# Kernel optimization log

Measured on AMD Instinct MI355X. Metric: run time of the kernel, lower is better.

The kernel has to match this reference:

```python
import jax, jax.numpy as jnp
import numpy as np

S, B, I, H = 512, 8192, 3, 5  # seq, batch, input_size, hidden_size


def _uniform(key, shape, bound):
    return jax.random.uniform(key, shape, jnp.float32, -bound, bound)


def setup_inputs() -> dict:
    key = jax.random.key(0)
    ks = jax.random.split(key, 17)
    bound = 1.0 / np.sqrt(H)
    inp = {"x": jax.random.normal(ks[0], (S, B, I), jnp.float32)}
    # layer 0: in=I ; layer 1: in=2H (concat of both directions). Suffix 'r' = reverse direction.
    specs = [
        ("l0", I), ("l0r", I), ("l1", 2 * H), ("l1r", 2 * H),
    ]
    ki = 1
    for name, din in specs:
        inp[f"w_ih_{name}"] = _uniform(ks[ki], (4 * H, din), bound); ki += 1
        inp[f"w_hh_{name}"] = _uniform(ks[ki], (4 * H, H), bound); ki += 1
        inp[f"b_ih_{name}"] = _uniform(ks[ki], (4 * H,), bound); ki += 1
        inp[f"b_hh_{name}"] = _uniform(ks[ki], (4 * H,), bound); ki += 1
    return inp


def _lstm_dir(x, w_ih, w_hh, b_ih, b_hh, reverse):
    """Single-direction LSTM over x [S,B,Din] -> (hs [S,B,H], h_T [B,H], c_T [B,H])."""
    xs = x[::-1] if reverse else x
    # Precompute input contributions for all timesteps in one big matmul.
    gx = jnp.einsum('sbi,gi->sbg', xs, w_ih) + b_ih + b_hh  # [S,B,4H]
    h0 = jnp.zeros((x.shape[1], H), x.dtype)
    c0 = jnp.zeros((x.shape[1], H), x.dtype)

    def step(carry, g):
        h, c = carry
        g = g + h @ w_hh.T  # [B,4H]
        i, f, gg, o = jnp.split(g, 4, axis=-1)  # PyTorch gate order: i,f,g,o
        i = jax.nn.sigmoid(i)
        f = jax.nn.sigmoid(f)
        gg = jnp.tanh(gg)
        o = jax.nn.sigmoid(o)
        c = f * c + i * gg
        h = o * jnp.tanh(c)
        return (h, c), h

    (hT, cT), hs = jax.lax.scan(step, (h0, c0), gx)
    if reverse:
        hs = hs[::-1]
    return hs, hT, cT


def reference(x,
              w_ih_l0, w_hh_l0, b_ih_l0, b_hh_l0,
              w_ih_l0r, w_hh_l0r, b_ih_l0r, b_hh_l0r,
              w_ih_l1, w_hh_l1, b_ih_l1, b_hh_l1,
              w_ih_l1r, w_hh_l1r, b_ih_l1r, b_hh_l1r):
    # Layer 0 (bidirectional)
    hs0f, h0f, c0f = _lstm_dir(x, w_ih_l0, w_hh_l0, b_ih_l0, b_hh_l0, False)
    hs0b, h0b, c0b = _lstm_dir(x, w_ih_l0r, w_hh_l0r, b_ih_l0r, b_hh_l0r, True)
    out0 = jnp.concatenate([hs0f, hs0b], axis=-1)  # [S,B,2H]
    # Layer 1 (bidirectional) consumes concat of both directions
    hs1f, h1f, c1f = _lstm_dir(out0, w_ih_l1, w_hh_l1, b_ih_l1, b_hh_l1, False)
    hs1b, h1b, c1b = _lstm_dir(out0, w_ih_l1r, w_hh_l1r, b_ih_l1r, b_hh_l1r, True)
    output = jnp.concatenate([hs1f, hs1b], axis=-1)  # [S,B,2H]
    # PyTorch h_n/c_n layout: [num_layers*num_directions, B, H] ordered (l0 fwd, l0 bwd, l1 fwd, l1 bwd)
    h_n = jnp.stack([h0f, h0b, h1f, h1b], axis=0)
    c_n = jnp.stack([c0f, c0b, c1f, c1b], axis=0)
    return output, h_n, c_n
```

## Files before the change

### kernel.cpp

```cpp
#include <hip/hip_runtime.h>


constexpr int S_ = 512;
constexpr int B_ = 8192;
constexpr int NROW = 16384;

constexpr float L2E  = 1.4426950408889634f;
constexpr float T2E  = 2.8853900817779268f;
constexpr float IT2E = 0.34657359027997264f;

typedef _Float16 v2h __attribute__((ext_vector_type(2)));

__device__ __forceinline__ float dot2h(v2h a, v2h b, float c) {
#if __has_builtin(__builtin_amdgcn_fdot2)
    return __builtin_amdgcn_fdot2(a, b, c, false);
#else
    return fmaf((float)a[0], (float)b[0], fmaf((float)a[1], (float)b[1], c));
#endif
}

__device__ __forceinline__ float rcp_(float x) { return __builtin_amdgcn_rcpf(x); }

__device__ __forceinline__ float exp2_(float x) {
#if __has_builtin(__builtin_amdgcn_exp2f)
    return __builtin_amdgcn_exp2f(x);
#else
    return exp2f(x);
#endif
}

__device__ __forceinline__ void sbar() { __builtin_amdgcn_sched_barrier(0); }

__device__ __forceinline__ float bperm(int bidx, float v) {
    return __int_as_float(__builtin_amdgcn_ds_bpermute(bidx, __float_as_int(v)));
}

__device__ __forceinline__ unsigned pkh(float a, float b) {
    auto t = __builtin_amdgcn_cvt_pkrtz(a, b);
    unsigned q; __builtin_memcpy(&q, &t, 4); return q;
}

__global__ __launch_bounds__(64) __attribute__((amdgpu_waves_per_eu(1, 2)))
void lstm_layer0(
    const float* __restrict__ x,
    const float* __restrict__ wih_f, const float* __restrict__ whh_f,
    const float* __restrict__ bih_f, const float* __restrict__ bhh_f,
    const float* __restrict__ wih_r, const float* __restrict__ whh_r,
    const float* __restrict__ bih_r, const float* __restrict__ bhh_r,
    unsigned short* __restrict__ ws,
    float* __restrict__ outbase)
{
    const int l64 = threadIdx.x & 63;
    int r = l64 / 5; r = (r > 11) ? 11 : r;
    const int u   = l64 - r * 5;
    const int uc  = (u < 5) ? u : 4;
    const int gid = blockIdx.x * 12 + r;
    const bool valid = gid < NROW;
    const int dir = (gid >> 13) & 1;
    const int b   = gid & 8191;
    const bool stw = valid && (u < 3);
    const bool st  = valid && (u < 5);

    int bidx[5];
#pragma unroll
    for (int k = 0; k < 5; k++) bidx[k] = (r * 5 + k) * 4;

    const float* __restrict__ wih = dir ? wih_r : wih_f;
    const float* __restrict__ whh = dir ? whh_r : whh_f;
    const float* __restrict__ bih = dir ? bih_r : bih_f;
    const float* __restrict__ bhh = dir ? bhh_r : bhh_f;

    const int rows[4] = {uc, 5 + uc, 10 + uc, 15 + uc};
    const float scl[4] = {-L2E, -L2E, T2E, -L2E};
    float WX[4][3], WH[4][5], BS[4];
#pragma unroll
    for (int gi = 0; gi < 4; gi++) {
        const int rr = rows[gi]; const float sc = scl[gi];
#pragma unroll
        for (int i = 0; i < 3; i++) WX[gi][i] = wih[rr * 3 + i] * sc;
#pragma unroll
        for (int k = 0; k < 5; k++) WH[gi][k] = whh[rr * 5 + k] * sc;
        BS[gi] = (bih[rr] + bhh[rr]) * sc;
    }

    float h[5] = {0.f, 0.f, 0.f, 0.f, 0.f};
    float cp = 0.f, hu_last = 0.f;

    const int t0 = dir ? (S_ - 1) : 0;
    const float* xp = x + ((size_t)t0 * B_ + b) * 3;
    unsigned short* wp = ws + (size_t)dir * ((size_t)S_ * B_ * 6)
                            + ((size_t)t0 * B_ + b) * 6;
    const ptrdiff_t xst = dir ? -(ptrdiff_t)3 * B_ : (ptrdiff_t)3 * B_;
    const ptrdiff_t wst = dir ? -(ptrdiff_t)6 * B_ : (ptrdiff_t)6 * B_;

    auto step = [&](const float (&xin)[3], unsigned short* wpp) {
        float a0 = BS[0], a1 = BS[1], a2 = BS[2], a3 = BS[3];
#pragma unroll
        for (int i = 0; i < 3; i++) {
            a0 = fmaf(WX[0][i], xin[i], a0);
            a1 = fmaf(WX[1][i], xin[i], a1);
            a2 = fmaf(WX[2][i], xin[i], a2);
            a3 = fmaf(WX[3][i], xin[i], a3);
        }
#pragma unroll
        for (int k = 0; k < 5; k++) {
            a0 = fmaf(WH[0][k], h[k], a0);
            a1 = fmaf(WH[1][k], h[k], a1);
            a2 = fmaf(WH[2][k], h[k], a2);
            a3 = fmaf(WH[3][k], h[k], a3);
        }
        const float ig = rcp_(1.0f + exp2_(a0));
        const float fg = rcp_(1.0f + exp2_(a1));
        const float g2 = fmaf(-2.0f * T2E, rcp_(1.0f + exp2_(a2)), T2E);
        const float og = rcp_(1.0f + exp2_(a3));
        cp = fmaf(fg, cp, ig * g2);
        const float th = fmaf(-2.0f, rcp_(1.0f + exp2_(cp)), 1.0f);
        const float hu = og * th;
        hu_last = hu;
#pragma unroll
        for (int k = 0; k < 5; k++) h[k] = bperm(bidx[k], hu);
        const unsigned q0 = pkh(h[0], h[1]);
        const unsigned q1 = pkh(h[2], h[3]);
        const unsigned q2 = pkh(h[4], 0.0f);
        unsigned qs = q0;
        qs = (u == 1) ? q1 : qs;
        qs = (u == 2) ? q2 : qs;
        if (stw) ((unsigned*)wpp)[u] = qs;
    };

    auto ld = [&](float (&buf)[3]) {
        __builtin_memcpy(&buf[0], xp, 12);
        xp += xst;
        sbar();
    };

    float x0[3], x1[3], x2[3], x3[3], x4[3], x5[3], x6[3], x7[3];
    ld(x0); ld(x1); ld(x2); ld(x3); ld(x4); ld(x5); ld(x6); ld(x7);

#pragma unroll 1
    for (int s = 0; s < S_ - 8; s += 8) {
        step(x0, wp); wp += wst; ld(x0);
        step(x1, wp); wp += wst; ld(x1);
        step(x2, wp); wp += wst; ld(x2);
        step(x3, wp); wp += wst; ld(x3);
        step(x4, wp); wp += wst; ld(x4);
        step(x5, wp); wp += wst; ld(x5);
        step(x6, wp); wp += wst; ld(x6);
        step(x7, wp); wp += wst; ld(x7);
    }
    step(x0, wp); wp += wst;
    step(x1, wp); wp += wst;
    step(x2, wp); wp += wst;
    step(x3, wp); wp += wst;
    step(x4, wp); wp += wst;
    step(x5, wp); wp += wst;
    step(x6, wp); wp += wst;
    step(x7, wp);

    const size_t OUTE = (size_t)S_ * B_ * 10;
    float* hn = outbase + OUTE + ((size_t)dir * B_ + b) * 5;
    float* cn = hn + (size_t)4 * B_ * 5;
    if (st) { hn[uc] = hu_last; cn[uc] = cp * IT2E; }
}

__global__ __launch_bounds__(64) __attribute__((amdgpu_waves_per_eu(1, 2)))
void lstm_layer1(
    const unsigned short* __restrict__ ws,
    const float* __restrict__ wih_f, const float* __restrict__ whh_f,
    const float* __restrict__ bih_f, const float* __restrict__ bhh_f,
    const float* __restrict__ wih_r, const float* __restrict__ whh_r,
    const float* __restrict__ bih_r, const float* __restrict__ bhh_r,
    float* __restrict__ outbase)
{
    const int l64 = threadIdx.x & 63;
    int r = l64 / 5; r = (r > 11) ? 11 : r;
    const int u   = l64 - r * 5;
    const int uc  = (u < 5) ? u : 4;
    const int gid = blockIdx.x * 12 + r;
    const bool valid = gid < NROW;
    const int dir = (gid >> 13) & 1;
    const int b   = gid & 8191;
    const bool st = valid && (u < 5);

    int bidx[5];
#pragma unroll
    for (int k = 0; k < 5; k++) bidx[k] = (r * 5 + k) * 4;

    const float* __restrict__ wih = dir ? wih_r : wih_f;
    const float* __restrict__ whh = dir ? whh_r : whh_f;
    const float* __restrict__ bih = dir ? bih_r : bih_f;
    const float* __restrict__ bhh = dir ? bhh_r : bhh_f;

    const int rows[4] = {uc, 5 + uc, 10 + uc, 15 + uc};
    const float scl[4] = {-L2E, -L2E, T2E, -L2E};
    v2h WX[4][6];
    float WH[4][5], BS[4];
#pragma unroll
    for (int gi = 0; gi < 4; gi++) {
        const int rr = rows[gi]; const float sc = scl[gi];
#pragma unroll
        for (int p = 0; p < 6; p++) {
            const int i0 = (p < 3) ? 2 * p : 2 * p - 1;
            const bool pad = (p == 2) || (p == 5);
            const float w0 = wih[rr * 10 + i0] * sc;
            const float w1 = pad ? 0.f : wih[rr * 10 + i0 + 1] * sc;
            WX[gi][p] = (v2h){(_Float16)w0, (_Float16)w1};
        }
#pragma unroll
        for (int k = 0; k < 5; k++) WH[gi][k] = whh[rr * 5 + k] * sc;
        BS[gi] = (bih[rr] + bhh[rr]) * sc;
    }

    float h[5] = {0.f, 0.f, 0.f, 0.f, 0.f};
    float cp = 0.f, hu_last = 0.f;

    const int t0 = dir ? (S_ - 1) : 0;
    const unsigned short* rpf = ws + ((size_t)t0 * B_ + b) * 6;
    const unsigned short* rpb = rpf + (size_t)S_ * B_ * 6;
    float* op = outbase + ((size_t)t0 * B_ + b) * 10 + dir * 5;
    const ptrdiff_t rst = dir ? -(ptrdiff_t)6 * B_ : (ptrdiff_t)6 * B_;
    const ptrdiff_t ost = dir ? -(ptrdiff_t)10 * B_ : (ptrdiff_t)10 * B_;

    auto step = [&](const v2h (&xin)[6], float* opp) {
        float a0 = BS[0], a1 = BS[1], a2 = BS[2], a3 = BS[3];
#pragma unroll
        for (int p = 0; p < 6; p++) {
            a0 = dot2h(xin[p], WX[0][p], a0);
            a1 = dot2h(xin[p], WX[1][p], a1);
            a2 = dot2h(xin[p], WX[2][p], a2);
            a3 = dot2h(xin[p], WX[3][p], a3);
        }
#pragma unroll
        for (int k = 0; k < 5; k++) {
            a0 = fmaf(WH[0][k], h[k], a0);
            a1 = fmaf(WH[1][k], h[k], a1);
            a2 = fmaf(WH[2][k], h[k], a2);
            a3 = fmaf(WH[3][k], h[k], a3);
        }
        const float ig = rcp_(1.0f + exp2_(a0));
        const float fg = rcp_(1.0f + exp2_(a1));
        const float g2 = fmaf(-2.0f * T2E, rcp_(1.0f + exp2_(a2)), T2E);
        const float og = rcp_(1.0f + exp2_(a3));
        cp = fmaf(fg, cp, ig * g2);
        const float th = fmaf(-2.0f, rcp_(1.0f + exp2_(cp)), 1.0f);
        const float hu = og * th;
        hu_last = hu;
        if (st) opp[u] = hu;
#pragma unroll
        for (int k = 0; k < 5; k++) h[k] = bperm(bidx[k], hu);
    };

    auto ld = [&](v2h (&buf)[6]) {
        __builtin_memcpy(&buf[0], rpf, 12);
        __builtin_memcpy(&buf[3], rpb, 12);
        rpf += rst; rpb += rst;
        sbar();
    };

    v2h x0[6], x1[6], x2[6], x3[6];
    ld(x0); ld(x1); ld(x2); ld(x3);

#pragma unroll 1
    for (int s = 0; s < S_ - 4; s += 4) {
        step(x0, op); op += ost; ld(x0);
        step(x1, op); op += ost; ld(x1);
        step(x2, op); op += ost; ld(x2);
        step(x3, op); op += ost; ld(x3);
    }
    step(x0, op); op += ost;
    step(x1, op); op += ost;
    step(x2, op); op += ost;
    step(x3, op);

    const size_t OUTE = (size_t)S_ * B_ * 10;
    float* hn = outbase + OUTE + ((size_t)(2 + dir) * B_ + b) * 5;
    float* cn = hn + (size_t)4 * B_ * 5;
    if (st) { hn[uc] = hu_last; cn[uc] = cp * IT2E; }
}

extern "C" void kernel_launch(void* const* d_in, const int* in_sizes, int n_in,
                              void* d_out, int out_size, void* d_ws, size_t ws_size,
                              hipStream_t stream) {
    const float* x       = (const float*)d_in[0];
    const float* wih_l0  = (const float*)d_in[1];
    const float* whh_l0  = (const float*)d_in[2];
    const float* bih_l0  = (const float*)d_in[3];
    const float* bhh_l0  = (const float*)d_in[4];
    const float* wih_l0r = (const float*)d_in[5];
    const float* whh_l0r = (const float*)d_in[6];
    const float* bih_l0r = (const float*)d_in[7];
    const float* bhh_l0r = (const float*)d_in[8];
    const float* wih_l1  = (const float*)d_in[9];
    const float* whh_l1  = (const float*)d_in[10];
    const float* bih_l1  = (const float*)d_in[11];
    const float* bhh_l1  = (const float*)d_in[12];
    const float* wih_l1r = (const float*)d_in[13];
    const float* whh_l1r = (const float*)d_in[14];
    const float* bih_l1r = (const float*)d_in[15];
    const float* bhh_l1r = (const float*)d_in[16];

    float* out = (float*)d_out;
    unsigned short* ws = (unsigned short*)d_ws;

    dim3 grid(1366), block(64);
    lstm_layer0<<<grid, block, 0, stream>>>(x,
        wih_l0, whh_l0, bih_l0, bhh_l0,
        wih_l0r, whh_l0r, bih_l0r, bhh_l0r,
        ws, out);
    lstm_layer1<<<grid, block, 0, stream>>>(ws,
        wih_l1, whh_l1, bih_l1, bhh_l1,
        wih_l1r, whh_l1r, bih_l1r, bhh_l1r,
        out);
}
```

Measured before the change: 325.2 us.

## Pair fwd/bwd layer-1 rows per block and write full 10-float output rows

Layer 1 now places the forward and backward directions of the same batch element in one wave. Each direction stashes its first 256 hidden outputs in LDS (fp16, 208 steps) or in a global spill buffer. It then writes complete 10-float output rows, both directions' halves, during the second half of the sequence. This replaces the strided 5-float half-row writes with contiguous full-row stores, which should improve write coalescing. The cost is LDS use, an extra global temp buffer, fp16 rounding of the stored half of the outputs, and extra per-step loads.

```diff
diff --git a/kernel.cpp b/kernel.cpp
--- a/kernel.cpp
+++ b/kernel.cpp
@@ -4,6 +4,10 @@
 constexpr int S_ = 512;
 constexpr int B_ = 8192;
 constexpr int NROW = 16384;
+
+constexpr int GD1  = 1366;
+constexpr int TL   = 208;
+constexpr int GSTR = GD1 * 64;
 
 constexpr float L2E  = 1.4426950408889634f;
 constexpr float T2E  = 2.8853900817779268f;
@@ -38,6 +42,15 @@
 __device__ __forceinline__ unsigned pkh(float a, float b) {
     auto t = __builtin_amdgcn_cvt_pkrtz(a, b);
     unsigned q; __builtin_memcpy(&q, &t, 4); return q;
+}
+
+__device__ __forceinline__ unsigned short f2h(float x) {
+    _Float16 h = (_Float16)x;
+    unsigned short s; __builtin_memcpy(&s, &h, 2); return s;
+}
+
+__device__ __forceinline__ float h2f(unsigned short s) {
+    _Float16 h; __builtin_memcpy(&h, &s, 2); return (float)h;
 }
 
 __global__ __launch_bounds__(64) __attribute__((amdgpu_waves_per_eu(1, 2)))
@@ -170,17 +183,24 @@
     const float* __restrict__ bih_f, const float* __restrict__ bhh_f,
     const float* __restrict__ wih_r, const float* __restrict__ whh_r,
     const float* __restrict__ bih_r, const float* __restrict__ bhh_r,
-    float* __restrict__ outbase)
+    float* __restrict__ outbase,
+    unsigned short* __restrict__ gtemp)
 {
+    __shared__ unsigned short lt[TL * 60];
+
     const int l64 = threadIdx.x & 63;
     int r = l64 / 5; r = (r > 11) ? 11 : r;
     const int u   = l64 - r * 5;
     const int uc  = (u < 5) ? u : 4;
-    const int gid = blockIdx.x * 12 + r;
-    const bool valid = gid < NROW;
-    const int dir = (gid >> 13) & 1;
-    const int b   = gid & 8191;
+    const int rm  = (r < 6) ? r : r - 6;
+    const int dir = (r >= 6) ? 1 : 0;
+    const int braw = blockIdx.x * 6 + rm;
+    const bool valid = braw < B_;
+    const int b   = valid ? braw : (B_ - 1);
     const bool st = valid && (u < 5);
+    const bool lw = (l64 < 60);
+    const int dir5 = dir * 5;
+    const int pslot = (dir ? (r - 6) : (r + 6)) * 5 + uc;
 
     int bidx[5];
 #pragma unroll
@@ -217,11 +237,15 @@
     const int t0 = dir ? (S_ - 1) : 0;
     const unsigned short* rpf = ws + ((size_t)t0 * B_ + b) * 6;
     const unsigned short* rpb = rpf + (size_t)S_ * B_ * 6;
-    float* op = outbase + ((size_t)t0 * B_ + b) * 10 + dir * 5;
+    float* op = outbase + ((size_t)(dir ? 255 : 256) * B_ + b) * 10;
     const ptrdiff_t rst = dir ? -(ptrdiff_t)6 * B_ : (ptrdiff_t)6 * B_;
     const ptrdiff_t ost = dir ? -(ptrdiff_t)10 * B_ : (ptrdiff_t)10 * B_;
 
-    auto step = [&](const v2h (&xin)[6], float* opp) {
+    unsigned short* gw = gtemp + (size_t)blockIdx.x * 64 + l64;
+    const unsigned short* gr = gtemp + (size_t)47 * GSTR
+                                     + (size_t)blockIdx.x * 64 + pslot;
+
+    auto core = [&](const v2h (&xin)[6]) -> float {
         float a0 = BS[0], a1 = BS[1], a2 = BS[2], a3 = BS[3];
 #pragma unroll
         for (int p = 0; p < 6; p++) {
@@ -245,9 +269,37 @@
         const float th = fmaf(-2.0f, rcp_(1.0f + exp2_(cp)), 1.0f);
         const float hu = og * th;
         hu_last = hu;
-        if (st) opp[u] = hu;
+        return hu;
+    };
+
+    auto bcast = [&](float hu) {
 #pragma unroll
         for (int k = 0; k < 5; k++) h[k] = bperm(bidx[k], hu);
+    };
+
+    auto step1L = [&](const v2h (&xin)[6], int t) {
+        const float hu = core(xin);
+        if (lw) lt[t * 60 + l64] = f2h(hu);
+        bcast(hu);
+    };
+    auto step1G = [&](const v2h (&xin)[6]) {
+        const float hu = core(xin);
+        *gw = f2h(hu);
+        gw += GSTR;
+        bcast(hu);
+    };
+    auto step2G = [&](const v2h (&xin)[6], float* opp) {
+        const float pv = h2f(*gr);
+        gr -= GSTR;
+        const float hu = core(xin);
+        if (st) { opp[dir5 + u] = hu; opp[5 - dir5 + u] = pv; }
+        bcast(hu);
+    };
+    auto step2L = [&](const v2h (&xin)[6], int t, float* opp) {
+        const float pv = h2f(lt[(511 - t) * 60 + pslot]);
+        const float hu = core(xin);
+        if (st) { opp[dir5 + u] = hu; opp[5 - dir5 + u] = pv; }
+        bcast(hu);
     };
 
     auto ld = [&](v2h (&buf)[6]) {
@@ -261,16 +313,37 @@
     ld(x0); ld(x1); ld(x2); ld(x3);
 
 #pragma unroll 1
-    for (int s = 0; s < S_ - 4; s += 4) {
-        step(x0, op); op += ost; ld(x0);
-        step(x1, op); op += ost; ld(x1);
-        step(x2, op); op += ost; ld(x2);
-        step(x3, op); op += ost; ld(x3);
-    }
-    step(x0, op); op += ost;
-    step(x1, op); op += ost;
-    step(x2, op); op += ost;
-    step(x3, op);
+    for (int t = 0; t < TL; t += 4) {
+        step1L(x0, t + 0); ld(x0);
+        step1L(x1, t + 1); ld(x1);
+        step1L(x2, t + 2); ld(x2);
+        step1L(x3, t + 3); ld(x3);
+    }
+#pragma unroll 1
+    for (int t = TL; t < 256; t += 4) {
+        step1G(x0); ld(x0);
+        step1G(x1); ld(x1);
+        step1G(x2); ld(x2);
+        step1G(x3); ld(x3);
+    }
+#pragma unroll 1
+    for (int t = 256; t < 304; t += 4) {
+        step2G(x0, op); op += ost; ld(x0);
+        step2G(x1, op); op += ost; ld(x1);
+        step2G(x2, op); op += ost; ld(x2);
+        step2G(x3, op); op += ost; ld(x3);
+    }
+#pragma unroll 1
+    for (int t = 304; t < 508; t += 4) {
+        step2L(x0, t + 0, op); op += ost; ld(x0);
+        step2L(x1, t + 1, op); op += ost; ld(x1);
+        step2L(x2, t + 2, op); op += ost; ld(x2);
+        step2L(x3, t + 3, op); op += ost; ld(x3);
+    }
+    step2L(x0, 508, op); op += ost;
+    step2L(x1, 509, op); op += ost;
+    step2L(x2, 510, op); op += ost;
+    step2L(x3, 511, op);
 
     const size_t OUTE = (size_t)S_ * B_ * 10;
     float* hn = outbase + OUTE + ((size_t)(2 + dir) * B_ + b) * 5;
@@ -301,14 +374,16 @@
 
     float* out = (float*)d_out;
     unsigned short* ws = (unsigned short*)d_ws;
-
-    dim3 grid(1366), block(64);
-    lstm_layer0<<<grid, block, 0, stream>>>(x,
+    unsigned short* gtemp = ws + (size_t)2 * S_ * B_ * 6;
+
+    dim3 grid0(1366), block(64);
+    lstm_layer0<<<grid0, block, 0, stream>>>(x,
         wih_l0, whh_l0, bih_l0, bhh_l0,
         wih_l0r, whh_l0r, bih_l0r, bhh_l0r,
         ws, out);
-    lstm_layer1<<<grid, block, 0, stream>>>(ws,
+    dim3 grid1(GD1);
+    lstm_layer1<<<grid1, block, 0, stream>>>(ws,
         wih_l1, whh_l1, bih_l1, bhh_l1,
         wih_l1r, whh_l1r, bih_l1r, bhh_l1r,
-        out);
-}
+        out, gtemp);
+}
```

Result: no change. 330.8 us (+1.7%).

## Remap layer-1 LSTM lanes to gate-parallel layout with fused bidirectional output staging

Applied to the files above, without the earlier changes.

Layer 1 now assigns each lane one gate (i, f, g or o) for five hidden units of a batch row, replacing the old mapping of one hidden unit per lane. Gates are exchanged with quad DPP broadcasts instead of ds_bpermute, and forward and reverse rows share a wave. Each direction stages its first-half hidden states as fp16 in LDS (with a global spill for the remainder) so the partner direction can write full 10-wide output rows in the second half. Block IDs for both kernels are also swizzled across XCDs. The aim is to cut cross-lane shuffle cost and scattered output stores, at the price of more register pressure, LDS use and fp16 rounding of the staged outputs.

```diff
diff --git a/kernel.cpp b/kernel.cpp
--- a/kernel.cpp
+++ b/kernel.cpp
@@ -4,6 +4,9 @@
 constexpr int S_ = 512;
 constexpr int B_ = 8192;
 constexpr int NROW = 16384;
+
+constexpr int GD1 = 1024;
+constexpr int TL  = 208;
 
 constexpr float L2E  = 1.4426950408889634f;
 constexpr float T2E  = 2.8853900817779268f;
@@ -35,9 +38,30 @@
     return __int_as_float(__builtin_amdgcn_ds_bpermute(bidx, __float_as_int(v)));
 }
 
+template<int L>
+__device__ __forceinline__ float qb(float v) {
+    return __int_as_float(__builtin_amdgcn_update_dpp(
+        0, __float_as_int(v), L * 0x55, 0xF, 0xF, false));
+}
+
 __device__ __forceinline__ unsigned pkh(float a, float b) {
     auto t = __builtin_amdgcn_cvt_pkrtz(a, b);
     unsigned q; __builtin_memcpy(&q, &t, 4); return q;
+}
+
+__device__ __forceinline__ unsigned short f2h(float x) {
+    _Float16 h = (_Float16)x;
+    unsigned short s; __builtin_memcpy(&s, &h, 2); return s;
+}
+
+__device__ __forceinline__ float h2f(unsigned short s) {
+    _Float16 h; __builtin_memcpy(&h, &s, 2); return (float)h;
+}
+
+__device__ __forceinline__ int xswz1366(int bid) {
+    const int xcd = bid & 7, loc = bid >> 3;
+    const int base = (xcd < 6) ? xcd * 171 : 1026 + (xcd - 6) * 170;
+    return base + loc;
 }
 
 __global__ __launch_bounds__(64) __attribute__((amdgpu_waves_per_eu(1, 2)))
@@ -54,7 +78,8 @@
     int r = l64 / 5; r = (r > 11) ? 11 : r;
     const int u   = l64 - r * 5;
     const int uc  = (u < 5) ? u : 4;
-    const int gid = blockIdx.x * 12 + r;
+    const int bsw = xswz1366((int)blockIdx.x);
+    const int gid = bsw * 12 + r;
     const bool valid = gid < NROW;
     const int dir = (gid >> 13) & 1;
     const int b   = gid & 8191;
@@ -170,85 +195,59 @@
     const float* __restrict__ bih_f, const float* __restrict__ bhh_f,
     const float* __restrict__ wih_r, const float* __restrict__ whh_r,
     const float* __restrict__ bih_r, const float* __restrict__ bhh_r,
-    float* __restrict__ outbase)
+    float* __restrict__ outbase,
+    unsigned short* __restrict__ gtemp)
 {
+    __shared__ unsigned lt[TL * 48];
+
     const int l64 = threadIdx.x & 63;
-    int r = l64 / 5; r = (r > 11) ? 11 : r;
-    const int u   = l64 - r * 5;
-    const int uc  = (u < 5) ? u : 4;
-    const int gid = blockIdx.x * 12 + r;
-    const bool valid = gid < NROW;
-    const int dir = (gid >> 13) & 1;
-    const int b   = gid & 8191;
-    const bool st = valid && (u < 5);
-
-    int bidx[5];
-#pragma unroll
-    for (int k = 0; k < 5; k++) bidx[k] = (r * 5 + k) * 4;
+    const int bid = (int)blockIdx.x;
+    const int bsw = (bid & 7) * 128 + (bid >> 3);
+    const int q   = l64 >> 2;
+    const int g   = l64 & 3;
+    const int dir = q >> 3;
+    const int qm  = q & 7;
+    const int b   = bsw * 8 + qm;
+    const int pq  = q ^ 8;
+    const bool c2sel = (g == 0) ? (dir == 0) : (dir == 1);
 
     const float* __restrict__ wih = dir ? wih_r : wih_f;
     const float* __restrict__ whh = dir ? whh_r : whh_f;
     const float* __restrict__ bih = dir ? bih_r : bih_f;
     const float* __restrict__ bhh = dir ? bhh_r : bhh_f;
 
-    const int rows[4] = {uc, 5 + uc, 10 + uc, 15 + uc};
-    const float scl[4] = {-L2E, -L2E, T2E, -L2E};
-    v2h WX[4][6];
-    float WH[4][5], BS[4];
-#pragma unroll
-    for (int gi = 0; gi < 4; gi++) {
-        const int rr = rows[gi]; const float sc = scl[gi];
+    const float scl = (g == 2) ? T2E : -L2E;
+    const float GM  = (g == 2) ? (-2.0f * T2E) : 1.0f;
+    const float GB  = (g == 2) ? T2E : 0.0f;
+
+    v2h  WX[5][6];
+    float WH[5][5], BS[5];
+#pragma unroll
+    for (int u = 0; u < 5; u++) {
+        const int rr = g * 5 + u;
 #pragma unroll
         for (int p = 0; p < 6; p++) {
             const int i0 = (p < 3) ? 2 * p : 2 * p - 1;
             const bool pad = (p == 2) || (p == 5);
-            const float w0 = wih[rr * 10 + i0] * sc;
-            const float w1 = pad ? 0.f : wih[rr * 10 + i0 + 1] * sc;
-            WX[gi][p] = (v2h){(_Float16)w0, (_Float16)w1};
-        }
-#pragma unroll
-        for (int k = 0; k < 5; k++) WH[gi][k] = whh[rr * 5 + k] * sc;
-        BS[gi] = (bih[rr] + bhh[rr]) * sc;
+            const float w0 = wih[rr * 10 + i0] * scl;
+            const float w1 = pad ? 0.f : wih[rr * 10 + i0 + 1] * scl;
+            WX[u][p] = (v2h){(_Float16)w0, (_Float16)w1};
+        }
+#pragma unroll
+        for (int k = 0; k < 5; k++) WH[u][k] = whh[rr * 5 + k] * scl;
+        BS[u] = (bih[rr] + bhh[rr]) * scl;
     }
 
-    float h[5] = {0.f, 0.f, 0.f, 0.f, 0.f};
-    float cp = 0.f, hu_last = 0.f;
+    float h[5]  = {0.f, 0.f, 0.f, 0.f, 0.f};
+    float cp[5] = {0.f, 0.f, 0.f, 0.f, 0.f};
 
     const int t0 = dir ? (S_ - 1) : 0;
     const unsigned short* rpf = ws + ((size_t)t0 * B_ + b) * 6;
     const unsigned short* rpb = rpf + (size_t)S_ * B_ * 6;
-    float* op = outbase + ((size_t)t0 * B_ + b) * 10 + dir * 5;
     const ptrdiff_t rst = dir ? -(ptrdiff_t)6 * B_ : (ptrdiff_t)6 * B_;
+    float* A  = outbase + ((size_t)(dir ? 255 : 256) * B_ + b) * 10 + g;
+    float* A2 = outbase + ((size_t)(dir ? 255 : 256) * B_ + b) * 10 + ((g == 0) ? 4 : 9);
     const ptrdiff_t ost = dir ? -(ptrdiff_t)10 * B_ : (ptrdiff_t)10 * B_;
-
-    auto step = [&](const v2h (&xin)[6], float* opp) {
-        float a0 = BS[0], a1 = BS[1], a2 = BS[2], a3 = BS[3];
-#pragma unroll
-        for (int p = 0; p < 6; p++) {
-            a0 = dot2h(xin[p], WX[0][p], a0);
-            a1 = dot2h(xin[p], WX[1][p], a1);
-            a2 = dot2h(xin[p], WX[2][p], a2);
-            a3 = dot2h(xin[p], WX[3][p], a3);
-        }
-#pragma unroll
-        for (int k = 0; k < 5; k++) {
-            a0 = fmaf(WH[0][k], h[k], a0);
-            a1 = fmaf(WH[1][k], h[k], a1);
-            a2 = fmaf(WH[2][k], h[k], a2);
-            a3 = fmaf(WH[3][k], h[k], a3);
-        }
-        const float ig = rcp_(1.0f + exp2_(a0));
-        const float fg = rcp_(1.0f + exp2_(a1));
-        const float g2 = fmaf(-2.0f * T2E, rcp_(1.0f + exp2_(a2)), T2E);
-        const float og = rcp_(1.0f + exp2_(a3));
-        cp = fmaf(fg, cp, ig * g2);
-        const float th = fmaf(-2.0f, rcp_(1.0f + exp2_(cp)), 1.0f);
-        const float hu = og * th;
-        hu_last = hu;
-        if (st) opp[u] = hu;
-#pragma unroll
-        for (int k = 0; k < 5; k++) h[k] = bperm(bidx[k], hu);
-    };
 
     auto ld = [&](v2h (&buf)[6]) {
         __builtin_memcpy(&buf[0], rpf, 12);
@@ -256,26 +255,112 @@
         rpf += rst; rpb += rst;
         sbar();
     };
+    auto dots = [&](const v2h (&xin)[6], float (&a)[5]) {
+#pragma unroll
+        for (int u = 0; u < 5; u++) {
+            float t = BS[u];
+#pragma unroll
+            for (int p = 0; p < 6; p++) t = dot2h(xin[p], WX[u][p], t);
+            a[u] = t;
+        }
+    };
+    auto finish = [&](float (&a)[5]) {
+#pragma unroll
+        for (int u = 0; u < 5; u++) {
+#pragma unroll
+            for (int k = 0; k < 5; k++) a[u] = fmaf(WH[u][k], h[k], a[u]);
+        }
+        float gv[5];
+#pragma unroll
+        for (int u = 0; u < 5; u++)
+            gv[u] = fmaf(GM, rcp_(1.0f + exp2_(a[u])), GB);
+#pragma unroll
+        for (int u = 0; u < 5; u++) {
+            const float ig = qb<0>(gv[u]);
+            const float fg = qb<1>(gv[u]);
+            const float gg = qb<2>(gv[u]);
+            const float og = qb<3>(gv[u]);
+            cp[u] = fmaf(fg, cp[u], ig * gg);
+            const float th = fmaf(-2.0f, rcp_(1.0f + exp2_(cp[u])), 1.0f);
+            h[u] = og * th;
+        }
+    };
+    auto hsel = [&]() -> float {
+        return (g == 0) ? h[0] : (g == 1) ? h[1] : (g == 2) ? h[2] : h[3];
+    };
+
+    unsigned* ltw = lt + q * 3 + g;
+    auto s1L = [&](v2h (&xb)[6]) {
+        float a[5]; dots(xb, a); ld(xb); finish(a);
+        const unsigned p0 = pkh(h[0], h[1]);
+        const unsigned p1 = pkh(h[2], h[3]);
+        const unsigned p2 = pkh(h[4], 0.0f);
+        unsigned qs = (g == 1) ? p1 : p0; qs = (g == 2) ? p2 : qs;
+        if (g < 3) *ltw = qs;
+        ltw += 48;
+    };
+    unsigned short* gsw = gtemp + (size_t)bid * (48 * 80) + q * 5 + g;
+    auto s1G = [&](v2h (&xb)[6]) {
+        float a[5]; dots(xb, a); ld(xb); finish(a);
+        *gsw = f2h(hsel());
+        if (g == 0) gsw[4] = f2h(h[4]);
+        gsw += 80;
+    };
+    auto outst = [&](float pvg, float pv4) {
+        const float hg = hsel();
+        A[0] = dir ? pvg : hg;
+        A[5] = dir ? hg : pvg;
+        if (g < 2) A2[0] = c2sel ? h[4] : pv4;
+        A += ost; A2 += ost;
+    };
+    const unsigned short* grd = gtemp + (size_t)bid * (48 * 80)
+                                      + (size_t)47 * 80 + pq * 5;
+    auto s2G = [&](v2h (&xb)[6]) {
+        const float pvg = h2f(grd[g]);
+        const float pv4 = h2f(grd[4]);
+        grd -= 80;
+        float a[5]; dots(xb, a); ld(xb); finish(a);
+        outst(pvg, pv4);
+    };
+    const unsigned short* lrd = (const unsigned short*)lt
+                              + (size_t)(TL - 1) * 96 + pq * 6;
+    auto s2L = [&](v2h (&xb)[6]) {
+        const float pvg = h2f(lrd[g]);
+        const float pv4 = h2f(lrd[4]);
+        lrd -= 96;
+        float a[5]; dots(xb, a); ld(xb); finish(a);
+        outst(pvg, pv4);
+    };
+    auto s2Ln = [&](v2h (&xb)[6]) {
+        const float pvg = h2f(lrd[g]);
+        const float pv4 = h2f(lrd[4]);
+        lrd -= 96;
+        float a[5]; dots(xb, a); finish(a);
+        outst(pvg, pv4);
+    };
 
     v2h x0[6], x1[6], x2[6], x3[6];
     ld(x0); ld(x1); ld(x2); ld(x3);
 
 #pragma unroll 1
-    for (int s = 0; s < S_ - 4; s += 4) {
-        step(x0, op); op += ost; ld(x0);
-        step(x1, op); op += ost; ld(x1);
-        step(x2, op); op += ost; ld(x2);
-        step(x3, op); op += ost; ld(x3);
-    }
-    step(x0, op); op += ost;
-    step(x1, op); op += ost;
-    step(x2, op); op += ost;
-    step(x3, op);
+    for (int t = 0; t < TL; t += 4) { s1L(x0); s1L(x1); s1L(x2); s1L(x3); }
+#pragma unroll 1
+    for (int t = TL; t < 256; t += 4) { s1G(x0); s1G(x1); s1G(x2); s1G(x3); }
+    asm volatile("s_waitcnt vmcnt(0)" ::: "memory");
+#pragma unroll 1
+    for (int t = 256; t < 304; t += 4) { s2G(x0); s2G(x1); s2G(x2); s2G(x3); }
+#pragma unroll 1
+    for (int t = 304; t < 508; t += 4) { s2L(x0); s2L(x1); s2L(x2); s2L(x3); }
+    s2Ln(x0); s2Ln(x1); s2Ln(x2); s2Ln(x3);
 
     const size_t OUTE = (size_t)S_ * B_ * 10;
     float* hn = outbase + OUTE + ((size_t)(2 + dir) * B_ + b) * 5;
     float* cn = hn + (size_t)4 * B_ * 5;
-    if (st) { hn[uc] = hu_last; cn[uc] = cp * IT2E; }
+    const float hg = hsel();
+    const float cg = ((g == 0) ? cp[0] : (g == 1) ? cp[1] :
+                      (g == 2) ? cp[2] : cp[3]) * IT2E;
+    hn[g] = hg; cn[g] = cg;
+    if (g == 0) { hn[4] = h[4]; cn[4] = cp[4] * IT2E; }
 }
 
 extern "C" void kernel_launch(void* const* d_in, const int* in_sizes, int n_in,
@@ -301,14 +386,16 @@
 
     float* out = (float*)d_out;
     unsigned short* ws = (unsigned short*)d_ws;
-
-    dim3 grid(1366), block(64);
-    lstm_layer0<<<grid, block, 0, stream>>>(x,
+    unsigned short* gtemp = ws + (size_t)2 * S_ * B_ * 6;
+
+    dim3 grid0(1366), block(64);
+    lstm_layer0<<<grid0, block, 0, stream>>>(x,
         wih_l0, whh_l0, bih_l0, bhh_l0,
         wih_l0r, whh_l0r, bih_l0r, bhh_l0r,
         ws, out);
-    lstm_layer1<<<grid, block, 0, stream>>>(ws,
+    dim3 grid1(GD1);
+    lstm_layer1<<<grid1, block, 0, stream>>>(ws,
         wih_l1, whh_l1, bih_l1, bhh_l1,
         wih_l1r, whh_l1r, bih_l1r, bhh_l1r,
-        out);
-}
+        out, gtemp);
+}
```

Measured after the change: 341.9 us. +5.2%, slower.

## Restructure layer-1 LSTM as paired-lane units with LDS-staged output interleave

Applied to the files above, without the earlier changes.

Layer 1 is remapped so each pair of lanes owns one (batch, direction) sequence. One lane computes the i/g gates and the other the f/o gates for all 5 hidden units, and they exchange values through a DPP swap instead of five ds_bpermute calls per step. Forward and reverse sequences for the same batch share a block. During the first half of the sequence, results are stashed in LDS (with a small global spill past 240 steps), so each lane can write a contiguous 20-byte row holding both directions' hidden state in the second half. This removes the 5-of-64 wasted-lane layout and the scattered 4-byte stores, at the cost of a large LDS footprint, more registers per lane, and a single wave per EU.

```diff
diff --git a/kernel.cpp b/kernel.cpp
--- a/kernel.cpp
+++ b/kernel.cpp
@@ -4,6 +4,9 @@
 constexpr int S_ = 512;
 constexpr int B_ = 8192;
 constexpr int NROW = 16384;
+
+constexpr int GD1 = 512;
+constexpr int TL1 = 240;
 
 constexpr float L2E  = 1.4426950408889634f;
 constexpr float T2E  = 2.8853900817779268f;
@@ -35,9 +38,23 @@
     return __int_as_float(__builtin_amdgcn_ds_bpermute(bidx, __float_as_int(v)));
 }
 
+__device__ __forceinline__ float dsw(float v) {
+    return __int_as_float(__builtin_amdgcn_update_dpp(
+        0, __float_as_int(v), 0xB1, 0xF, 0xF, false));
+}
+
 __device__ __forceinline__ unsigned pkh(float a, float b) {
     auto t = __builtin_amdgcn_cvt_pkrtz(a, b);
     unsigned q; __builtin_memcpy(&q, &t, 4); return q;
+}
+
+__device__ __forceinline__ unsigned short f2h(float x) {
+    _Float16 h = (_Float16)x;
+    unsigned short s; __builtin_memcpy(&s, &h, 2); return s;
+}
+
+__device__ __forceinline__ float h2f(unsigned short s) {
+    _Float16 h; __builtin_memcpy(&h, &s, 2); return (float)h;
 }
 
 __global__ __launch_bounds__(64) __attribute__((amdgpu_waves_per_eu(1, 2)))
@@ -163,92 +180,74 @@
     if (st) { hn[uc] = hu_last; cn[uc] = cp * IT2E; }
 }
 
-__global__ __launch_bounds__(64) __attribute__((amdgpu_waves_per_eu(1, 2)))
+__global__ __launch_bounds__(64) __attribute__((amdgpu_waves_per_eu(1)))
 void lstm_layer1(
     const unsigned short* __restrict__ ws,
     const float* __restrict__ wih_f, const float* __restrict__ whh_f,
     const float* __restrict__ bih_f, const float* __restrict__ bhh_f,
     const float* __restrict__ wih_r, const float* __restrict__ whh_r,
     const float* __restrict__ bih_r, const float* __restrict__ bhh_r,
-    float* __restrict__ outbase)
+    float* __restrict__ outbase,
+    unsigned short* __restrict__ gtemp)
 {
+    __shared__ unsigned       ltA[TL1 * 64];
+    __shared__ unsigned short ltB[TL1 * 32];
+
     const int l64 = threadIdx.x & 63;
-    int r = l64 / 5; r = (r > 11) ? 11 : r;
-    const int u   = l64 - r * 5;
-    const int uc  = (u < 5) ? u : 4;
-    const int gid = blockIdx.x * 12 + r;
-    const bool valid = gid < NROW;
-    const int dir = (gid >> 13) & 1;
-    const int b   = gid & 8191;
-    const bool st = valid && (u < 5);
-
-    int bidx[5];
-#pragma unroll
-    for (int k = 0; k < 5; k++) bidx[k] = (r * 5 + k) * 4;
+    const int bid = (int)blockIdx.x;
+    const int bsw = (bid & 7) * 64 + (bid >> 3);
+    const int par = l64 & 1;
+    const int k   = l64 >> 1;
+    const int dir = k >> 4;
+    const int b   = bsw * 16 + (k & 15);
+    const int pk  = k ^ 16;
 
     const float* __restrict__ wih = dir ? wih_r : wih_f;
     const float* __restrict__ whh = dir ? whh_r : whh_f;
     const float* __restrict__ bih = dir ? bih_r : bih_f;
     const float* __restrict__ bhh = dir ? bhh_r : bhh_f;
 
-    const int rows[4] = {uc, 5 + uc, 10 + uc, 15 + uc};
-    const float scl[4] = {-L2E, -L2E, T2E, -L2E};
-    v2h WX[4][6];
-    float WH[4][5], BS[4];
-#pragma unroll
-    for (int gi = 0; gi < 4; gi++) {
-        const int rr = rows[gi]; const float sc = scl[gi];
-#pragma unroll
-        for (int p = 0; p < 6; p++) {
-            const int i0 = (p < 3) ? 2 * p : 2 * p - 1;
-            const bool pad = (p == 2) || (p == 5);
-            const float w0 = wih[rr * 10 + i0] * sc;
-            const float w1 = pad ? 0.f : wih[rr * 10 + i0 + 1] * sc;
-            WX[gi][p] = (v2h){(_Float16)w0, (_Float16)w1};
-        }
-#pragma unroll
-        for (int k = 0; k < 5; k++) WH[gi][k] = whh[rr * 5 + k] * sc;
-        BS[gi] = (bih[rr] + bhh[rr]) * sc;
-    }
-
-    float h[5] = {0.f, 0.f, 0.f, 0.f, 0.f};
-    float cp = 0.f, hu_last = 0.f;
+    const int G0 = par ? 2 : 0, G1 = par ? 3 : 1;
+    const float s0 = par ? T2E : -L2E;
+    const float GM0 = par ? (-2.0f * T2E) : 1.0f;
+    const float GB0 = par ? T2E : 0.0f;
+
+    v2h  WX[10][6];
+    float WH[10][5], BS[10];
+#pragma unroll
+    for (int u = 0; u < 5; u++) {
+        const int rr0 = G0 * 5 + u, rr1 = G1 * 5 + u;
+#pragma unroll
+        for (int q = 0; q < 6; q++) {
+            const int i0 = (q < 3) ? 2 * q : 2 * q - 1;
+            const bool pad = (q == 2) || (q == 5);
+            const float a0 = wih[rr0 * 10 + i0] * s0;
+            const float a1 = pad ? 0.f : wih[rr0 * 10 + i0 + 1] * s0;
+            WX[u][q] = (v2h){(_Float16)a0, (_Float16)a1};
+            const float b0 = wih[rr1 * 10 + i0] * (-L2E);
+            const float b1 = pad ? 0.f : wih[rr1 * 10 + i0 + 1] * (-L2E);
+            WX[5 + u][q] = (v2h){(_Float16)b0, (_Float16)b1};
+        }
+#pragma unroll
+        for (int kk = 0; kk < 5; kk++) {
+            WH[u][kk]     = whh[rr0 * 5 + kk] * s0;
+            WH[5 + u][kk] = whh[rr1 * 5 + kk] * (-L2E);
+        }
+        BS[u]     = (bih[rr0] + bhh[rr0]) * s0;
+        BS[5 + u] = (bih[rr1] + bhh[rr1]) * (-L2E);
+    }
+
+    float h[5]  = {0.f, 0.f, 0.f, 0.f, 0.f};
+    float cp[5] = {0.f, 0.f, 0.f, 0.f, 0.f};
 
     const int t0 = dir ? (S_ - 1) : 0;
     const unsigned short* rpf = ws + ((size_t)t0 * B_ + b) * 6;
     const unsigned short* rpb = rpf + (size_t)S_ * B_ * 6;
-    float* op = outbase + ((size_t)t0 * B_ + b) * 10 + dir * 5;
     const ptrdiff_t rst = dir ? -(ptrdiff_t)6 * B_ : (ptrdiff_t)6 * B_;
+    float* op = outbase + ((size_t)(dir ? 255 : 256) * B_ + b) * 10
+                        + (par ? (5 - dir * 5) : dir * 5);
     const ptrdiff_t ost = dir ? -(ptrdiff_t)10 * B_ : (ptrdiff_t)10 * B_;
-
-    auto step = [&](const v2h (&xin)[6], float* opp) {
-        float a0 = BS[0], a1 = BS[1], a2 = BS[2], a3 = BS[3];
-#pragma unroll
-        for (int p = 0; p < 6; p++) {
-            a0 = dot2h(xin[p], WX[0][p], a0);
-            a1 = dot2h(xin[p], WX[1][p], a1);
-            a2 = dot2h(xin[p], WX[2][p], a2);
-            a3 = dot2h(xin[p], WX[3][p], a3);
-        }
-#pragma unroll
-        for (int k = 0; k < 5; k++) {
-            a0 = fmaf(WH[0][k], h[k], a0);
-            a1 = fmaf(WH[1][k], h[k], a1);
-            a2 = fmaf(WH[2][k], h[k], a2);
-            a3 = fmaf(WH[3][k], h[k], a3);
-        }
-        const float ig = rcp_(1.0f + exp2_(a0));
-        const float fg = rcp_(1.0f + exp2_(a1));
-        const float g2 = fmaf(-2.0f * T2E, rcp_(1.0f + exp2_(a2)), T2E);
-        const float og = rcp_(1.0f + exp2_(a3));
-        cp = fmaf(fg, cp, ig * g2);
-        const float th = fmaf(-2.0f, rcp_(1.0f + exp2_(cp)), 1.0f);
-        const float hu = og * th;
-        hu_last = hu;
-        if (st) opp[u] = hu;
-#pragma unroll
-        for (int k = 0; k < 5; k++) h[k] = bperm(bidx[k], hu);
-    };
+    unsigned short* gsp = gtemp + (size_t)bid * (16 * 160);
 
     auto ld = [&](v2h (&buf)[6]) {
         __builtin_memcpy(&buf[0], rpf, 12);
@@ -257,25 +256,121 @@
         sbar();
     };
 
+    float A[10];
+    auto dots = [&](const v2h (&xin)[6]) {
+#pragma unroll
+        for (int j = 0; j < 10; j++) {
+            float t = BS[j];
+#pragma unroll
+            for (int q = 0; q < 6; q++) t = dot2h(xin[q], WX[j][q], t);
+            A[j] = t;
+        }
+    };
+    auto finish = [&]() {
+#pragma unroll
+        for (int j = 0; j < 10; j++) {
+#pragma unroll
+            for (int kk = 0; kk < 5; kk++) A[j] = fmaf(WH[j][kk], h[kk], A[j]);
+        }
+        float v0[5], v1[5], z0[5], z1[5];
+#pragma unroll
+        for (int u = 0; u < 5; u++) {
+            v0[u] = fmaf(GM0, rcp_(1.0f + exp2_(A[u])), GB0);
+            v1[u] = rcp_(1.0f + exp2_(A[5 + u]));
+        }
+#pragma unroll
+        for (int u = 0; u < 5; u++) { z0[u] = dsw(v0[u]); z1[u] = dsw(v1[u]); }
+#pragma unroll
+        for (int u = 0; u < 5; u++) {
+            const float F = par ? z1[u] : v1[u];
+            const float O = par ? v1[u] : z1[u];
+            cp[u] = fmaf(F, cp[u], v0[u] * z0[u]);
+            const float th = fmaf(-2.0f, rcp_(1.0f + exp2_(cp[u])), 1.0f);
+            h[u] = O * th;
+        }
+    };
+
+    auto outst = [&](float p0, float p1, float p2, float p3, float p4) {
+        float buf[5];
+        buf[0] = par ? p0 : h[0];
+        buf[1] = par ? p1 : h[1];
+        buf[2] = par ? p2 : h[2];
+        buf[3] = par ? p3 : h[3];
+        buf[4] = par ? p4 : h[4];
+        __builtin_memcpy(op, buf, 20);
+        op += ost;
+    };
+
+    auto s1L = [&](v2h (&xb)[6], int t) {
+        dots(xb); ld(xb); finish();
+        const unsigned d = par ? pkh(h[2], h[3]) : pkh(h[0], h[1]);
+        ltA[t * 64 + l64] = d;
+        if (!par) ltB[t * 32 + k] = f2h(h[4]);
+    };
+    auto s1G = [&](v2h (&xb)[6], int tp) {
+        dots(xb); ld(xb); finish();
+        const unsigned d = par ? pkh(h[2], h[3]) : pkh(h[0], h[1]);
+        __builtin_memcpy(gsp + (size_t)tp * 160 + l64 * 2, &d, 4);
+        if (!par) gsp[(size_t)tp * 160 + 128 + k] = f2h(h[4]);
+    };
+    auto s2G = [&](v2h (&xb)[6], int tp) {
+        unsigned two[2];
+        __builtin_memcpy(two, gsp + (size_t)tp * 160 + pk * 4, 8);
+        const unsigned short s4 = gsp[(size_t)tp * 160 + 128 + pk];
+        dots(xb); ld(xb); finish();
+        v2h t01, t23;
+        __builtin_memcpy(&t01, &two[0], 4); __builtin_memcpy(&t23, &two[1], 4);
+        outst((float)t01[0], (float)t01[1], (float)t23[0], (float)t23[1], h2f(s4));
+    };
+    auto s2L = [&](v2h (&xb)[6], int tau) {
+        const unsigned d01 = ltA[tau * 64 + 2 * pk];
+        const unsigned d23 = ltA[tau * 64 + 2 * pk + 1];
+        const unsigned short s4 = ltB[tau * 32 + pk];
+        dots(xb); ld(xb); finish();
+        v2h t01, t23;
+        __builtin_memcpy(&t01, &d01, 4); __builtin_memcpy(&t23, &d23, 4);
+        outst((float)t01[0], (float)t01[1], (float)t23[0], (float)t23[1], h2f(s4));
+    };
+    auto s2Ln = [&](v2h (&xb)[6], int tau) {
+        const unsigned d01 = ltA[tau * 64 + 2 * pk];
+        const unsigned d23 = ltA[tau * 64 + 2 * pk + 1];
+        const unsigned short s4 = ltB[tau * 32 + pk];
+        dots(xb); finish();
+        v2h t01, t23;
+        __builtin_memcpy(&t01, &d01, 4); __builtin_memcpy(&t23, &d23, 4);
+        outst((float)t01[0], (float)t01[1], (float)t23[0], (float)t23[1], h2f(s4));
+    };
+
     v2h x0[6], x1[6], x2[6], x3[6];
     ld(x0); ld(x1); ld(x2); ld(x3);
 
 #pragma unroll 1
-    for (int s = 0; s < S_ - 4; s += 4) {
-        step(x0, op); op += ost; ld(x0);
-        step(x1, op); op += ost; ld(x1);
-        step(x2, op); op += ost; ld(x2);
-        step(x3, op); op += ost; ld(x3);
-    }
-    step(x0, op); op += ost;
-    step(x1, op); op += ost;
-    step(x2, op); op += ost;
-    step(x3, op);
+    for (int t = 0; t < TL1; t += 4) {
+        s1L(x0, t + 0); s1L(x1, t + 1); s1L(x2, t + 2); s1L(x3, t + 3);
+    }
+#pragma unroll 1
+    for (int t = TL1; t < 256; t += 4) {
+        s1G(x0, t - 240); s1G(x1, t - 239); s1G(x2, t - 238); s1G(x3, t - 237);
+    }
+    asm volatile("s_waitcnt vmcnt(0)" ::: "memory");
+#pragma unroll 1
+    for (int t = 256; t < 272; t += 4) {
+        s2G(x0, 271 - t); s2G(x1, 270 - t); s2G(x2, 269 - t); s2G(x3, 268 - t);
+    }
+#pragma unroll 1
+    for (int t = 272; t < 508; t += 4) {
+        s2L(x0, 511 - t); s2L(x1, 510 - t); s2L(x2, 509 - t); s2L(x3, 508 - t);
+    }
+    s2Ln(x0, 3); s2Ln(x1, 2); s2Ln(x2, 1); s2Ln(x3, 0);
 
     const size_t OUTE = (size_t)S_ * B_ * 10;
     float* hn = outbase + OUTE + ((size_t)(2 + dir) * B_ + b) * 5;
     float* cn = hn + (size_t)4 * B_ * 5;
-    if (st) { hn[uc] = hu_last; cn[uc] = cp * IT2E; }
+    float* ep = par ? cn : hn;
+    float eb[5];
+#pragma unroll
+    for (int u = 0; u < 5; u++) eb[u] = par ? cp[u] * IT2E : h[u];
+    __builtin_memcpy(ep, eb, 20);
 }
 
 extern "C" void kernel_launch(void* const* d_in, const int* in_sizes, int n_in,
@@ -301,14 +396,16 @@
 
     float* out = (float*)d_out;
     unsigned short* ws = (unsigned short*)d_ws;
-
-    dim3 grid(1366), block(64);
-    lstm_layer0<<<grid, block, 0, stream>>>(x,
+    unsigned short* gtemp = ws + (size_t)2 * S_ * B_ * 6;
+
+    dim3 grid0(1366), block(64);
+    lstm_layer0<<<grid0, block, 0, stream>>>(x,
         wih_l0, whh_l0, bih_l0, bhh_l0,
         wih_l0r, whh_l0r, bih_l0r, bhh_l0r,
         ws, out);
-    lstm_layer1<<<grid, block, 0, stream>>>(ws,
+    dim3 grid1(GD1);
+    lstm_layer1<<<grid1, block, 0, stream>>>(ws,
         wih_l1, whh_l1, bih_l1, bhh_l1,
         wih_l1r, whh_l1r, bih_l1r, bhh_l1r,
-        out);
-}
+        out, gtemp);
+}
```

After: 439.0 us. 35.0% more time.
